# Optimization experiments

Measured on AMD Instinct MI355X. Metric: run time of the kernel, lower is better.

Reference implementation:

```python
import jax, jax.numpy as jnp
import numpy as np

DIM = 512  # module's self.dim, used for the softmax scale (note: NOT head dim)

def setup_inputs() -> dict:
    key = jax.random.key(0)
    kq, kk, kv = jax.random.split(key, 3)
    shape = (4, 8, 2048, 64)  # [B, H, S, Dh]
    q = jax.random.normal(kq, shape, dtype=jnp.float32)
    k = jax.random.normal(kk, shape, dtype=jnp.float32)
    v = jax.random.normal(kv, shape, dtype=jnp.float32)
    return {"q": q, "k": k, "v": v, "n": 2048}

def reference(q, k, v, n):
    # scores = q @ k^T, then divide by sqrt(dim) AFTER matmul (as in source)
    scores = jnp.einsum('bhqd,bhkd->bhqk', q, k)
    scale = jnp.sqrt(jnp.asarray(DIM, dtype=scores.dtype))
    p_attn = jax.nn.softmax(scores / scale, axis=-1)
    return jnp.einsum('bhqk,bhkd->bhqd', p_attn, v)
```

## Files before the change

### kernel.cpp

```cpp
#include <hip/hip_runtime.h>


using half8  = __attribute__((ext_vector_type(8))) _Float16;
using half4  = __attribute__((ext_vector_type(4))) _Float16;
using half2v = __attribute__((ext_vector_type(2))) _Float16;
using f32x4  = __attribute__((ext_vector_type(4))) float;

static __device__ __forceinline__ half2v cvt_pk(float a, float b) {
    return __builtin_bit_cast(half2v, __builtin_amdgcn_cvt_pkrtz(a, b));
}

#define SEQ   2048
#define DH    64
#define QB    128
#define KVB   64
#define NKVT  (SEQ / KVB)
#define NQB   (SEQ / QB)
#define QSCALE (1.4426950408889634f / 22.627416997969522f)

#if __has_builtin(__builtin_amdgcn_exp2f)
#define EXP2F __builtin_amdgcn_exp2f
#else
#define EXP2F exp2f
#endif

#define GLOAD4(dst, ptr) \
    asm volatile("global_load_dwordx4 %0, %1, off" : "=v"(dst) : "v"(ptr) : "memory")

#define WAIT_VM0()                                            \
    do {                                                      \
        asm volatile("s_waitcnt vmcnt(0)" ::: "memory");      \
        __builtin_amdgcn_sched_barrier(0);                    \
    } while (0)

#define LDS_BARRIER()                                         \
    do {                                                      \
        asm volatile("s_waitcnt lgkmcnt(0)" ::: "memory");    \
        __builtin_amdgcn_s_barrier();                         \
    } while (0)

__global__ __launch_bounds__(256, 2)
void fattn_fwd(const float* __restrict__ Qg, const float* __restrict__ Kg,
               const float* __restrict__ Vg, float* __restrict__ Og)
{
    __shared__ __align__(16) _Float16 Klds[2][KVB * DH];
    __shared__ __align__(16) _Float16 VTlds[2][DH * KVB];
    __shared__ __align__(16) _Float16 Plds[4 * 32 * KVB];

    const int tid  = threadIdx.x;
    const int lane = tid & 63;
    const int wave = tid >> 6;
    const int l16  = lane & 15;
    const int lg   = lane >> 4;

    const int wg  = blockIdx.x;
    const int swz = (wg & 7) * 64 + (wg >> 3);
    const int qb  = swz & (NQB - 1);
    const int bh  = swz >> 4;
    const size_t base = (size_t)bh * (SEQ * DH);

    half8 qfrag[2][2];
#pragma unroll
    for (int qs = 0; qs < 2; ++qs) {
        const int qrow = qb * QB + wave * 32 + qs * 16 + l16;
        const float* qp = Qg + base + (size_t)qrow * DH + lg * 8;
#pragma unroll
        for (int ks = 0; ks < 2; ++ks) {
            f32x4 a = *(const f32x4*)(qp + ks * 32);
            f32x4 b = *(const f32x4*)(qp + ks * 32 + 4);
            half8 f;
#pragma unroll
            for (int i = 0; i < 4; ++i) f[i]     = (_Float16)(a[i] * QSCALE);
#pragma unroll
            for (int i = 0; i < 4; ++i) f[i + 4] = (_Float16)(b[i] * QSCALE);
            qfrag[qs][ks] = f;
        }
    }

    f32x4 acc[2][4];
    float lsum[2][4];
#pragma unroll
    for (int qs = 0; qs < 2; ++qs)
#pragma unroll
        for (int r = 0; r < 4; ++r) {
            lsum[qs][r] = 0.f;
            acc[qs][r] = f32x4{0.f, 0.f, 0.f, 0.f};
        }

    char* pbase = (char*)(Plds + wave * (32 * KVB));

    f32x4 kreg[4];
    f32x4 vreg[4];

    auto load_tile = [&](int kvt) {
        const float* kg = Kg + base + (size_t)kvt * (KVB * DH);
        const float* vg = Vg + base + (size_t)kvt * (KVB * DH);
#pragma unroll
        for (int it = 0; it < 4; ++it) {
            int row = it * 16 + (tid >> 4);
            GLOAD4(kreg[it], kg + (size_t)row * DH + (tid & 15) * 4);
        }
#pragma unroll
        for (int it = 0; it < 2; ++it) {
            int kv = (tid & 31) * 2;
            int d0 = (it * 8 + (tid >> 5)) * 4;
            GLOAD4(vreg[it * 2 + 0], vg + (size_t)kv * DH + d0);
            GLOAD4(vreg[it * 2 + 1], vg + (size_t)(kv + 1) * DH + d0);
        }
    };

    auto write_tile = [&](int b) {
        char* kb = (char*)Klds[b];
        char* vb = (char*)VTlds[b];
#pragma unroll
        for (int it = 0; it < 4; ++it) {
            int row  = it * 16 + (tid >> 4);
            int byte = (row * 128 + (tid & 15) * 8) ^ ((row & 7) << 4);
            f32x4 a  = kreg[it];
            half2v lo = cvt_pk(a[0], a[1]);
            half2v hi = cvt_pk(a[2], a[3]);
            half4 h;
            h[0] = lo[0]; h[1] = lo[1]; h[2] = hi[0]; h[3] = hi[1];
            *(half4*)(kb + byte) = h;
        }
#pragma unroll
        for (int it = 0; it < 2; ++it) {
            int kv = (tid & 31) * 2;
            int d0 = (it * 8 + (tid >> 5)) * 4;
            f32x4 a = vreg[it * 2 + 0];
            f32x4 c = vreg[it * 2 + 1];
#pragma unroll
            for (int i = 0; i < 4; ++i) {
                int row  = d0 + i;
                int byte = (row * 128 + kv * 2) ^ ((row & 7) << 4);
                *(half2v*)(vb + byte) = cvt_pk(a[i], c[i]);
            }
        }
    };

    load_tile(0);
    WAIT_VM0();
    write_tile(0);

    for (int kvt = 0; kvt < NKVT; ++kvt) {
        const int cur = kvt & 1;
        char* kbase = (char*)Klds[cur];
        char* vbase = (char*)VTlds[cur];

        if (kvt + 1 < NKVT) load_tile(kvt + 1);

        LDS_BARRIER();

        half8 kf[4][2];
#pragma unroll
        for (int kvs = 0; kvs < 4; ++kvs)
#pragma unroll
            for (int ks = 0; ks < 2; ++ks) {
                int row  = kvs * 16 + l16;
                int byte = (row * 128 + ks * 64 + lg * 16) ^ ((row & 7) << 4);
                kf[kvs][ks] = *(const half8*)(kbase + byte);
            }
        f32x4 s[2][4];
        __builtin_amdgcn_s_setprio(1);
#pragma unroll
        for (int qs = 0; qs < 2; ++qs)
#pragma unroll
            for (int kvs = 0; kvs < 4; ++kvs) {
                f32x4 c = f32x4{0.f, 0.f, 0.f, 0.f};
#pragma unroll
                for (int ks = 0; ks < 2; ++ks)
                    c = __builtin_amdgcn_mfma_f32_16x16x32_f16(
                            qfrag[qs][ks], kf[kvs][ks], c, 0, 0, 0);
                s[qs][kvs] = c;
            }
        __builtin_amdgcn_s_setprio(0);

#pragma unroll
        for (int qs = 0; qs < 2; ++qs)
#pragma unroll
            for (int kvs = 0; kvs < 4; ++kvs)
#pragma unroll
                for (int r = 0; r < 4; ++r) {
                    float p = EXP2F(s[qs][kvs][r]);
                    lsum[qs][r] += p;
                    int row  = qs * 16 + lg * 4 + r;
                    int col  = kvs * 16 + l16;
                    int byte = (row * 128 + col * 2) ^ ((row & 7) << 4);
                    *(_Float16*)(pbase + byte) = (_Float16)p;
                }

#pragma unroll
        for (int ks = 0; ks < 2; ++ks) {
            half8 vf[4];
#pragma unroll
            for (int d = 0; d < 4; ++d) {
                int vrow  = d * 16 + l16;
                int vbyte = (vrow * 128 + ks * 64 + lg * 16) ^ ((vrow & 7) << 4);
                vf[d] = *(const half8*)(vbase + vbyte);
            }
            __builtin_amdgcn_s_setprio(1);
#pragma unroll
            for (int qs = 0; qs < 2; ++qs) {
                int prow  = qs * 16 + l16;
                int pbyte = (prow * 128 + ks * 64 + lg * 16) ^ ((prow & 7) << 4);
                half8 pf  = *(const half8*)(pbase + pbyte);
#pragma unroll
                for (int d = 0; d < 4; ++d)
                    acc[qs][d] = __builtin_amdgcn_mfma_f32_16x16x32_f16(
                                     pf, vf[d], acc[qs][d], 0, 0, 0);
            }
            __builtin_amdgcn_s_setprio(0);
        }

        if (kvt + 1 < NKVT) {
            WAIT_VM0();
            write_tile(cur ^ 1);
        }
    }

#pragma unroll
    for (int qs = 0; qs < 2; ++qs)
#pragma unroll
        for (int r = 0; r < 4; ++r) {
            float t = lsum[qs][r];
            t += __shfl_xor(t, 1);
            t += __shfl_xor(t, 2);
            t += __shfl_xor(t, 4);
            t += __shfl_xor(t, 8);
            float invl = 1.f / t;
            int orow = qb * QB + wave * 32 + qs * 16 + lg * 4 + r;
            float* op = Og + base + (size_t)orow * DH;
#pragma unroll
            for (int d = 0; d < 4; ++d)
                op[d * 16 + l16] = acc[qs][d][r] * invl;
        }
}

extern "C" void kernel_launch(void* const* d_in, const int* in_sizes, int n_in,
                              void* d_out, int out_size, void* d_ws, size_t ws_size,
                              hipStream_t stream) {
    const float* q = (const float*)d_in[0];
    const float* k = (const float*)d_in[1];
    const float* v = (const float*)d_in[2];
    float* o = (float*)d_out;
    fattn_fwd<<<dim3(NQB * 32, 1, 1), dim3(256, 1, 1), 0, stream>>>(q, k, v, o);
}
```

Measured before the change: 66.41 us.

## Pre-convert K/V to swizzled fp16 tile images in workspace for attention

Adds two prep kernels that convert K and V to fp16, transpose V, and write pre-swizzled 16KB tile images to the workspace. The attention kernel then streams each tile with plain 16-byte loads and copies it straight into LDS, with no conversion or scatter. This halves the bytes each of the 16 query blocks reads per KV tile and removes redundant conversion work. The cost is two extra launches plus a workspace write and read. It also swaps the QK^T MFMA operand order so each lane holds four consecutive columns, which allows packed half4 P stores and a simpler row-sum reduction. The old kernel is kept as a fallback when the workspace is too small.

```diff
diff --git a/kernel.cpp b/kernel.cpp
--- a/kernel.cpp
+++ b/kernel.cpp
@@ -5,6 +5,7 @@
 using half4  = __attribute__((ext_vector_type(4))) _Float16;
 using half2v = __attribute__((ext_vector_type(2))) _Float16;
 using f32x4  = __attribute__((ext_vector_type(4))) float;
+using ushort8 = __attribute__((ext_vector_type(8))) unsigned short;
 
 static __device__ __forceinline__ half2v cvt_pk(float a, float b) {
     return __builtin_bit_cast(half2v, __builtin_amdgcn_cvt_pkrtz(a, b));
@@ -16,6 +17,9 @@
 #define KVB   64
 #define NKVT  (SEQ / KVB)
 #define NQB   (SEQ / QB)
+#define NBH   32
+#define TILE_IMG_BYTES 16384
+#define WS_NEED ((size_t)NBH * NKVT * TILE_IMG_BYTES)
 #define QSCALE (1.4426950408889634f / 22.627416997969522f)
 
 #if __has_builtin(__builtin_amdgcn_exp2f)
@@ -39,12 +43,64 @@
         __builtin_amdgcn_s_barrier();                         \
     } while (0)
 
+__global__ __launch_bounds__(256)
+void prep_k(const float* __restrict__ Kg, char* __restrict__ ws)
+{
+    int id   = blockIdx.x * 256 + threadIdx.x;
+    int col4 = id & 15;
+    int row  = (id >> 4) & 63;
+    int kvt  = (id >> 10) & 31;
+    int bh   = id >> 15;
+    f32x4 v = *(const f32x4*)(Kg + ((size_t)(bh * SEQ) + kvt * 64 + row) * DH + col4 * 4);
+    half2v lo = cvt_pk(v[0], v[1]);
+    half2v hi = cvt_pk(v[2], v[3]);
+    half4 h; h[0] = lo[0]; h[1] = lo[1]; h[2] = hi[0]; h[3] = hi[1];
+    char* out = ws + (size_t)(bh * 32 + kvt) * TILE_IMG_BYTES
+                   + ((row * 128 + col4 * 8) ^ ((row & 7) << 4));
+    *(half4*)out = h;
+}
+
+__global__ __launch_bounds__(256)
+void prep_v(const float* __restrict__ Vg, char* __restrict__ ws)
+{
+    __shared__ unsigned short VT[64][72];
+    int bid = blockIdx.x;
+    int bh  = bid >> 5;
+    int kvt = bid & 31;
+    int tid = threadIdx.x;
+
+    const float* vg = Vg + (size_t)(bh * SEQ) * DH + (size_t)(kvt * 64) * DH;
+#pragma unroll
+    for (int rr = 0; rr < 4; ++rr) {
+        int kv = rr * 16 + (tid >> 4);
+        int d4 = (tid & 15) * 4;
+        f32x4 v = *(const f32x4*)(vg + (size_t)kv * DH + d4);
+#pragma unroll
+        for (int j = 0; j < 4; ++j)
+            VT[d4 + j][kv] = __builtin_bit_cast(unsigned short, (_Float16)v[j]);
+    }
+    __syncthreads();
+
+    int d   = tid >> 2;
+    int seg = tid & 3;
+    ushort8 h0, h1;
+#pragma unroll
+    for (int j = 0; j < 16; ++j) {
+        int off = seg * 32 + j * 2;
+        int kv  = (off ^ ((d & 7) << 4)) >> 1;
+        unsigned short val = VT[d][kv];
+        if (j < 8) h0[j] = val; else h1[j - 8] = val;
+    }
+    char* out = ws + (size_t)(bh * 32 + kvt) * TILE_IMG_BYTES + 8192 + d * 128 + seg * 32;
+    *(ushort8*)(out)      = h0;
+    *(ushort8*)(out + 16) = h1;
+}
+
 __global__ __launch_bounds__(256, 2)
-void fattn_fwd(const float* __restrict__ Qg, const float* __restrict__ Kg,
-               const float* __restrict__ Vg, float* __restrict__ Og)
+void fattn_fwd(const float* __restrict__ Qg, const char* __restrict__ Wimg,
+               float* __restrict__ Og)
 {
-    __shared__ __align__(16) _Float16 Klds[2][KVB * DH];
-    __shared__ __align__(16) _Float16 VTlds[2][DH * KVB];
+    __shared__ __align__(16) char KVl[2][TILE_IMG_BYTES];
     __shared__ __align__(16) _Float16 Plds[4 * 32 * KVB];
 
     const int tid  = threadIdx.x;
@@ -78,6 +134,170 @@
     }
 
     f32x4 acc[2][4];
+    float lsum[2] = {0.f, 0.f};
+#pragma unroll
+    for (int qs = 0; qs < 2; ++qs)
+#pragma unroll
+        for (int d = 0; d < 4; ++d) acc[qs][d] = f32x4{0.f, 0.f, 0.f, 0.f};
+
+    char* pbase = (char*)(Plds + wave * (32 * KVB));
+
+    const char* imgbase = Wimg + (size_t)(bh * 32) * TILE_IMG_BYTES;
+
+    f32x4 kreg[4];
+    auto load_tile = [&](int kvt) {
+        const char* img = imgbase + (size_t)kvt * TILE_IMG_BYTES;
+#pragma unroll
+        for (int it = 0; it < 4; ++it)
+            GLOAD4(kreg[it], img + it * 4096 + tid * 16);
+    };
+    auto write_tile = [&](int b) {
+        char* dst = KVl[b];
+#pragma unroll
+        for (int it = 0; it < 4; ++it)
+            *(f32x4*)(dst + it * 4096 + tid * 16) = kreg[it];
+    };
+
+    load_tile(0);
+    WAIT_VM0();
+    write_tile(0);
+
+    for (int kvt = 0; kvt < NKVT; ++kvt) {
+        const int cur = kvt & 1;
+        const char* kbase = KVl[cur];
+        const char* vbase = KVl[cur] + 8192;
+
+        if (kvt + 1 < NKVT) load_tile(kvt + 1);
+
+        LDS_BARRIER();
+
+        half8 kf[4][2];
+#pragma unroll
+        for (int kvs = 0; kvs < 4; ++kvs)
+#pragma unroll
+            for (int ks = 0; ks < 2; ++ks) {
+                int row  = kvs * 16 + l16;
+                int byte = (row * 128 + ks * 64 + lg * 16) ^ ((row & 7) << 4);
+                kf[kvs][ks] = *(const half8*)(kbase + byte);
+            }
+        f32x4 st[2][4];
+        __builtin_amdgcn_s_setprio(1);
+#pragma unroll
+        for (int qs = 0; qs < 2; ++qs)
+#pragma unroll
+            for (int kvs = 0; kvs < 4; ++kvs) {
+                f32x4 c = f32x4{0.f, 0.f, 0.f, 0.f};
+#pragma unroll
+                for (int ks = 0; ks < 2; ++ks)
+                    c = __builtin_amdgcn_mfma_f32_16x16x32_f16(
+                            kf[kvs][ks], qfrag[qs][ks], c, 0, 0, 0);
+                st[qs][kvs] = c;
+            }
+        __builtin_amdgcn_s_setprio(0);
+
+#pragma unroll
+        for (int qs = 0; qs < 2; ++qs)
+#pragma unroll
+            for (int kvs = 0; kvs < 4; ++kvs) {
+                float p0 = EXP2F(st[qs][kvs][0]);
+                float p1 = EXP2F(st[qs][kvs][1]);
+                float p2 = EXP2F(st[qs][kvs][2]);
+                float p3 = EXP2F(st[qs][kvs][3]);
+                lsum[qs] += (p0 + p1) + (p2 + p3);
+                half2v lo = cvt_pk(p0, p1);
+                half2v hi = cvt_pk(p2, p3);
+                half4 h; h[0] = lo[0]; h[1] = lo[1]; h[2] = hi[0]; h[3] = hi[1];
+                int row  = qs * 16 + l16;
+                int col  = kvs * 16 + lg * 4;
+                int byte = (row * 128 + col * 2) ^ ((row & 7) << 4);
+                *(half4*)(pbase + byte) = h;
+            }
+
+#pragma unroll
+        for (int ks = 0; ks < 2; ++ks) {
+            half8 vf[4];
+#pragma unroll
+            for (int d = 0; d < 4; ++d) {
+                int vrow  = d * 16 + l16;
+                int vbyte = (vrow * 128 + ks * 64 + lg * 16) ^ ((vrow & 7) << 4);
+                vf[d] = *(const half8*)(vbase + vbyte);
+            }
+            __builtin_amdgcn_s_setprio(1);
+#pragma unroll
+            for (int qs = 0; qs < 2; ++qs) {
+                int prow  = qs * 16 + l16;
+                int pbyte = (prow * 128 + ks * 64 + lg * 16) ^ ((prow & 7) << 4);
+                half8 pf  = *(const half8*)(pbase + pbyte);
+#pragma unroll
+                for (int d = 0; d < 4; ++d)
+                    acc[qs][d] = __builtin_amdgcn_mfma_f32_16x16x32_f16(
+                                     pf, vf[d], acc[qs][d], 0, 0, 0);
+            }
+            __builtin_amdgcn_s_setprio(0);
+        }
+
+        if (kvt + 1 < NKVT) {
+            WAIT_VM0();
+            write_tile(cur ^ 1);
+        }
+    }
+
+#pragma unroll
+    for (int qs = 0; qs < 2; ++qs) {
+        float t = lsum[qs];
+        t += __shfl_xor(t, 16);
+        t += __shfl_xor(t, 32);
+#pragma unroll
+        for (int r = 0; r < 4; ++r) {
+            float invl = 1.f / __shfl(t, lg * 4 + r);
+            int orow = qb * QB + wave * 32 + qs * 16 + lg * 4 + r;
+            float* op = Og + base + (size_t)orow * DH;
+#pragma unroll
+            for (int d = 0; d < 4; ++d)
+                op[d * 16 + l16] = acc[qs][d][r] * invl;
+        }
+    }
+}
+
+__global__ __launch_bounds__(256, 2)
+void fattn_fwd_v5(const float* __restrict__ Qg, const float* __restrict__ Kg,
+                  const float* __restrict__ Vg, float* __restrict__ Og)
+{
+    __shared__ __align__(16) _Float16 Klds[2][KVB * DH];
+    __shared__ __align__(16) _Float16 VTlds[2][DH * KVB];
+    __shared__ __align__(16) _Float16 Plds[4 * 32 * KVB];
+
+    const int tid  = threadIdx.x;
+    const int lane = tid & 63;
+    const int wave = tid >> 6;
+    const int l16  = lane & 15;
+    const int lg   = lane >> 4;
+
+    const int wg  = blockIdx.x;
+    const int swz = (wg & 7) * 64 + (wg >> 3);
+    const int qb  = swz & (NQB - 1);
+    const int bh  = swz >> 4;
+    const size_t base = (size_t)bh * (SEQ * DH);
+
+    half8 qfrag[2][2];
+#pragma unroll
+    for (int qs = 0; qs < 2; ++qs) {
+        const int qrow = qb * QB + wave * 32 + qs * 16 + l16;
+        const float* qp = Qg + base + (size_t)qrow * DH + lg * 8;
+#pragma unroll
+        for (int ks = 0; ks < 2; ++ks) {
+            f32x4 a = *(const f32x4*)(qp + ks * 32);
+            f32x4 b = *(const f32x4*)(qp + ks * 32 + 4);
+            half8 f;
+#pragma unroll
+            for (int i = 0; i < 4; ++i) f[i]     = (_Float16)(a[i] * QSCALE);
+#pragma unroll
+            for (int i = 0; i < 4; ++i) f[i + 4] = (_Float16)(b[i] * QSCALE);
+            qfrag[qs][ks] = f;
+        }
+    }
+
+    f32x4 acc[2][4];
     float lsum[2][4];
 #pragma unroll
     for (int qs = 0; qs < 2; ++qs)
@@ -88,7 +308,6 @@
         }
 
     char* pbase = (char*)(Plds + wave * (32 * KVB));
-
     f32x4 kreg[4];
     f32x4 vreg[4];
 
@@ -108,7 +327,6 @@
             GLOAD4(vreg[it * 2 + 1], vg + (size_t)(kv + 1) * DH + d0);
         }
     };
-
     auto write_tile = [&](int b) {
         char* kb = (char*)Klds[b];
         char* vb = (char*)VTlds[b];
@@ -119,8 +337,7 @@
             f32x4 a  = kreg[it];
             half2v lo = cvt_pk(a[0], a[1]);
             half2v hi = cvt_pk(a[2], a[3]);
-            half4 h;
-            h[0] = lo[0]; h[1] = lo[1]; h[2] = hi[0]; h[3] = hi[1];
+            half4 h; h[0] = lo[0]; h[1] = lo[1]; h[2] = hi[0]; h[3] = hi[1];
             *(half4*)(kb + byte) = h;
         }
 #pragma unroll
@@ -146,9 +363,7 @@
         const int cur = kvt & 1;
         char* kbase = (char*)Klds[cur];
         char* vbase = (char*)VTlds[cur];
-
         if (kvt + 1 < NKVT) load_tile(kvt + 1);
-
         LDS_BARRIER();
 
         half8 kf[4][2];
@@ -243,5 +458,12 @@
     const float* k = (const float*)d_in[1];
     const float* v = (const float*)d_in[2];
     float* o = (float*)d_out;
-    fattn_fwd<<<dim3(NQB * 32, 1, 1), dim3(256, 1, 1), 0, stream>>>(q, k, v, o);
-}
+    if (ws_size >= WS_NEED) {
+        char* ws = (char*)d_ws;
+        prep_k<<<dim3(4096, 1, 1), dim3(256, 1, 1), 0, stream>>>(k, ws);
+        prep_v<<<dim3(1024, 1, 1), dim3(256, 1, 1), 0, stream>>>(v, ws);
+        fattn_fwd<<<dim3(NQB * NBH, 1, 1), dim3(256, 1, 1), 0, stream>>>(q, ws, o);
+    } else {
+        fattn_fwd_v5<<<dim3(NQB * NBH, 1, 1), dim3(256, 1, 1), 0, stream>>>(q, k, v, o);
+    }
+}
```

Result: no change. 66.14 us (-0.4%).
